# Kernel tuning notes

Hardware: AMD Instinct MI355X
Metric: run time of the kernel (lower is better)

## Reference

```python
import jax, jax.numpy as jnp
import numpy as np

B, D, H, C, T = 65536, 512, 256, 100, 10
EPS = 0.01  # halt_epsilon


def setup_inputs() -> dict:
    key = jax.random.key(0)
    ks = jax.random.split(key, 10)
    sD = 1.0 / np.sqrt(D)
    sH = 1.0 / np.sqrt(H)
    return {
        "x": jax.random.normal(ks[0], (B, D), dtype=jnp.float32),
        # GRUCell params (PyTorch layout: rows chunked as [r; z; n])
        "W_ih": jax.random.uniform(ks[1], (3 * H, D), minval=-sD, maxval=sD, dtype=jnp.float32),
        "W_hh": jax.random.uniform(ks[2], (3 * H, H), minval=-sH, maxval=sH, dtype=jnp.float32),
        "b_ih": jax.random.uniform(ks[3], (3 * H,), minval=-sH, maxval=sH, dtype=jnp.float32),
        "b_hh": jax.random.uniform(ks[4], (3 * H,), minval=-sH, maxval=sH, dtype=jnp.float32),
        # halting unit
        "W_halt": jax.random.uniform(ks[5], (1, H), minval=-sH, maxval=sH, dtype=jnp.float32),
        "b_halt": jax.random.uniform(ks[6], (1,), minval=-sH, maxval=sH, dtype=jnp.float32),
        # readout
        "W_ro": jax.random.uniform(ks[7], (C, H), minval=-sH, maxval=sH, dtype=jnp.float32),
        "b_ro": jax.random.uniform(ks[8], (C,), minval=-sH, maxval=sH, dtype=jnp.float32),
    }


def _act_forward(x, W_ih, W_hh, b_ih, b_hh, W_halt, b_halt, W_ro, b_ro):
    dt = x.dtype
    thresh = jnp.asarray(1.0 - EPS, dt)
    # x is static across ponder steps -> precompute input projection once
    x_proj = x @ W_ih.T + b_ih                       # [B, 3H]
    xr, xz, xn = jnp.split(x_proj, 3, axis=-1)

    def step(carry, _):
        h, cum, rem, nup, acc = carry
        h_proj = h @ W_hh.T + b_hh                   # [B, 3H]
        hr, hz, hn = jnp.split(h_proj, 3, axis=-1)
        r = jax.nn.sigmoid(xr + hr)
        z = jax.nn.sigmoid(xz + hz)
        n = jnp.tanh(xn + r * hn)
        h_new = (1.0 - z) * n + z * h                # GRUCell update
        halt = jax.nn.sigmoid(h_new @ W_halt.T + b_halt)[:, 0]  # [B]
        logits_t = h_new @ W_ro.T + b_ro             # [B, C]
        still = (cum < thresh).astype(dt)
        new_halt = halt * still
        would = (cum + new_halt > thresh).astype(dt)
        remainder = (1.0 - cum) * would * still
        step_w = new_halt * (1.0 - would) + remainder
        cum2 = cum + step_w
        acc2 = acc + step_w[:, None] * h_new
        return (h_new, cum2, rem + remainder, nup + still, acc2), (h_new, halt, logits_t)

    zB = jnp.zeros((x.shape[0],), dt)
    init = (jnp.zeros((x.shape[0], W_hh.shape[1]), dt), zB, zB, zB,
            jnp.zeros((x.shape[0], W_hh.shape[1]), dt))
    (h, cum, remainders, n_updates, acc), (h_seq, halt_seq, logits_seq) = jax.lax.scan(
        step, init, None, length=T)
    logits = acc @ W_ro.T + b_ro                     # [B, C]
    ponder_cost = n_updates.mean() + remainders.mean()
    # scan stacks on axis 0 (time) -> move to dim 1 as torch.stack(dim=1)
    h_seq = jnp.swapaxes(h_seq, 0, 1)                # [B, T, H]
    halt_seq = jnp.swapaxes(halt_seq, 0, 1)          # [B, T]
    logits_seq = jnp.swapaxes(logits_seq, 0, 1)      # [B, T, C]
    return logits, ponder_cost, n_updates, h_seq, halt_seq, logits_seq


def reference(x, W_ih, W_hh, b_ih, b_hh, W_halt, b_halt, W_ro, b_ro):
    return _act_forward(x, W_ih, W_hh, b_ih, b_hh, W_halt, b_halt, W_ro, b_ro)
```

## Files before the change

kernel.cpp:

```cpp
#include <hip/hip_runtime.h>
#include <cmath>


namespace {
constexpr int B = 65536, D = 512, H = 256, C = 100, T = 10;

constexpr long OUT_LOGITS = 0;
constexpr long OUT_PONDER = (long)B * C;
constexpr long OUT_NUP    = OUT_PONDER + 1;
constexpr long OUT_HSEQ   = OUT_NUP + B;
constexpr long OUT_HALT   = OUT_HSEQ + (long)B * T * H;
constexpr long OUT_LSEQ   = OUT_HALT + (long)B * T;

constexpr long NIH  = 768L * D;
constexpr long NHH  = 768L * H;
constexpr long NAUG = 112L * H;

constexpr long WS_XP   = 0;
constexpr long WS_W16  = WS_XP + (long)B * 768;
constexpr long W_HALV  = 2 * (NIH + NHH + NAUG);
constexpr long WS_HL   = WS_W16 + (W_HALV + 1) / 2;
constexpr long WS_HP4  = WS_HL + (long)B * T;
constexpr long WS_NUPB = WS_HP4 + 4L * B * T;
constexpr long WS_REMB = WS_NUPB + B;
constexpr long WS_H16  = WS_REMB + B;
constexpr long H16_PER_T = 1024L * 32768;

constexpr float SC  = 256.f;
constexpr float ISC = 1.f / 256.f;
constexpr float SB  = 1.f / 65536.f;
}

typedef __attribute__((ext_vector_type(8))) _Float16 h8;
typedef __attribute__((ext_vector_type(4))) _Float16 h4;
typedef __attribute__((ext_vector_type(4))) float f4;

#define MFMA16(A, Bo, Cc) __builtin_amdgcn_mfma_f32_16x16x32_f16(A, Bo, Cc, 0, 0, 0)
#define PROD3(a, Ah, Al, Bh, Bl)                                               \
  a = MFMA16(Al, Bh, a);                                                       \
  a = MFMA16(Ah, Bl, a);                                                       \
  a = MFMA16(Ah, Bh, a);

__device__ __forceinline__ float sigmoidf_(float x) {
  if (x >= 0.f) { return 1.f / (1.f + expf(-x)); }
  float e = expf(x);
  return e / (1.f + e);
}

__device__ __forceinline__ void gload_lds16(const _Float16* g, _Float16* l) {
  __builtin_amdgcn_global_load_lds(
      (const __attribute__((address_space(1))) unsigned int*)g,
      (__attribute__((address_space(3))) unsigned int*)l, 16, 0, 0);
}

__global__ void k_prep(const float* __restrict__ wih_s, const float* __restrict__ whh_s,
                       const float* __restrict__ wro, const float* __restrict__ whalt,
                       _Float16* __restrict__ wr) {
  long idx = (long)blockIdx.x * 256 + threadIdx.x;
  if (idx < NIH) {
    float xs = wih_s[idx] * SC;
    _Float16 h = (_Float16)xs;
    _Float16 l = (_Float16)(xs - (float)h);
    wr[idx] = h; wr[NIH + idx] = l;
  }
  if (idx < NHH) {
    float xs = whh_s[idx] * SC;
    _Float16 h = (_Float16)xs;
    _Float16 l = (_Float16)(xs - (float)h);
    long b = 2 * NIH;
    wr[b + idx] = h; wr[b + NHH + idx] = l;
  }
  if (idx < NAUG) {
    int row = (int)(idx >> 8), k = (int)(idx & 255);
    float x = (row < C) ? wro[row * 256 + k] : ((row == C) ? whalt[k] : 0.f);
    float xs = x * SC;
    _Float16 h = (_Float16)xs;
    _Float16 l = (_Float16)(xs - (float)h);
    long b = 2 * (NIH + NHH);
    wr[b + idx] = h; wr[b + NAUG + idx] = l;
  }
}

__device__ __forceinline__ void stageA16(const float* __restrict__ src,
                                         _Float16* As0, _Float16* As1,
                                         int o) {
#pragma unroll
  for (int i = 0; i < 4; ++i) {
    float4 v = ((const float4*)src)[i];
    float vv[4] = {v.x, v.y, v.z, v.w};
    h4 hh, ll;
#pragma unroll
    for (int c = 0; c < 4; ++c) {
      float sv = vv[c] * SC;
      _Float16 h = (_Float16)sv;
      hh[c] = h;
      ll[c] = (_Float16)(sv - (float)h);
    }
    *(h4*)&As0[o + i * 4] = hh;
    *(h4*)&As1[o + i * 4] = ll;
  }
}

__global__ __launch_bounds__(256, 3) void k_xproj(
    const float* __restrict__ x, const _Float16* __restrict__ wih,
    const float* __restrict__ b_ih, float* __restrict__ xpt) {
  __shared__ __align__(16) _Float16 As0[128 * 40], As1[128 * 40];
  __shared__ __align__(16) _Float16 Bs[2][192 * 32];
  const int tid = threadIdx.x;
  const int w = tid >> 6, l = tid & 63;
  const int lr = l & 15, lq = l >> 4;
  const int bid = blockIdx.x;
  const int gid = (bid & 7) * 256 + (bid >> 3);
  const int c0 = (gid & 3) * 64;
  const int rb = (gid >> 2) * 128;

  f4 acc[8][3];
#pragma unroll
  for (int i = 0; i < 8; ++i)
#pragma unroll
    for (int g = 0; g < 3; ++g) acc[i][g] = (f4)0.f;

  for (int kc = 0; kc < 16; ++kc) {
    const int k0 = kc * 32;
    __syncthreads();
    {
      const int row = tid >> 1, kk0 = (tid & 1) * 16;
      stageA16(x + (long)(rb + row) * D + k0 + kk0, As0, As1, row * 40 + kk0);
    }
#pragma unroll
    for (int j = 0; j < 6; ++j) {
      int chunk = w * 6 + j;
      int plane = chunk / 12;
      int rem = chunk - plane * 12;
      int scol = rem * 16 + (l >> 2);
      int kq = l & 3;
      int gcol = (scol >> 6) * 256 + c0 + (scol & 63);
      gload_lds16(wih + (long)plane * NIH + (long)gcol * D + k0 + kq * 8,
                  &Bs[plane][rem * 512]);
    }
    __syncthreads();
    h8 Bh[3], Bl[3];
#pragma unroll
    for (int g = 0; g < 3; ++g) {
      Bh[g] = *(const h8*)&Bs[0][(g * 64 + w * 16 + lr) * 32 + lq * 8];
      Bl[g] = *(const h8*)&Bs[1][(g * 64 + w * 16 + lr) * 32 + lq * 8];
    }
#pragma unroll
    for (int i = 0; i < 8; ++i) {
      h8 Ah = *(const h8*)&As0[(i * 16 + lr) * 40 + lq * 8];
      h8 Al = *(const h8*)&As1[(i * 16 + lr) * 40 + lq * 8];
#pragma unroll
      for (int g = 0; g < 3; ++g) { PROD3(acc[i][g], Ah, Al, Bh[g], Bl[g]); }
    }
  }
  const int ch = c0 + w * 16 + lr;
  const int strip = gid & 3;
  float bi[3] = {b_ih[ch], b_ih[256 + ch], b_ih[512 + ch]};
  const long xoff = (long)(lq * 256 + w * 64 + lr * 4);
#pragma unroll
  for (int i = 0; i < 8; ++i) {
    const long t4s = (long)((gid >> 2) * 2 + (i >> 2)) * 4 + strip;
#pragma unroll
    for (int g = 0; g < 3; ++g) {
      float4 v = make_float4(fmaf(acc[i][g][0], SB, bi[g]),
                             fmaf(acc[i][g][1], SB, bi[g]),
                             fmaf(acc[i][g][2], SB, bi[g]),
                             fmaf(acc[i][g][3], SB, bi[g]));
      *(float4*)&xpt[((t4s * 3 + g) * 4 + (i & 3)) * 1024 + xoff] = v;
    }
  }
}

__global__ __launch_bounds__(256, 4) void k_gru(
    const _Float16* __restrict__ whh, const float* __restrict__ xpt,
    const float* __restrict__ b_hh, const float* __restrict__ w_halt,
    float* __restrict__ out, _Float16* __restrict__ h16,
    float* __restrict__ hp4, int t) {
  __shared__ __align__(16) char uSmem[32768];
  _Float16* AsBuf = (_Float16*)uSmem;
  float*    hseqS = (float*)uSmem;
  _Float16* h16S  = (_Float16*)(uSmem + 16384);
  __shared__ float lds_hp[64][4];
  const int tid = threadIdx.x;
  const int w = tid >> 6, l = tid & 63;
  const int lr = l & 15, lq = l >> 4;
  const int bid = blockIdx.x;
  const int gid = (bid & 7) * 512 + (bid >> 3);
  const int strip = gid & 3;
  const int c0 = strip * 64;
  const int rb = (gid >> 2) * 64;
  const long tilebase = (long)(rb >> 6) * 32768;
  const int ch = c0 + w * 16 + lr;
  const int kc_h = ch >> 5;

  const float bhr = b_hh[ch], bhz = b_hh[256 + ch], bhn = b_hh[512 + ch];
  const float whv = w_halt[ch];

  f4 acc[4][3];
  float ho[4][4];
  float xnv[4][4];
  const long t4s = (long)(gid >> 2) * 4 + strip;
  const long xoff = (long)(lq * 256 + w * 64 + lr * 4);
#pragma unroll
  for (int i = 0; i < 4; ++i) {
    float4 vr = *(const float4*)&xpt[((t4s * 3 + 0) * 4 + i) * 1024 + xoff];
    float4 vz = *(const float4*)&xpt[((t4s * 3 + 1) * 4 + i) * 1024 + xoff];
    float4 vn = *(const float4*)&xpt[((t4s * 3 + 2) * 4 + i) * 1024 + xoff];
    acc[i][0][0] = vr.x * 65536.f; acc[i][0][1] = vr.y * 65536.f;
    acc[i][0][2] = vr.z * 65536.f; acc[i][0][3] = vr.w * 65536.f;
    acc[i][1][0] = vz.x * 65536.f; acc[i][1][1] = vz.y * 65536.f;
    acc[i][1][2] = vz.z * 65536.f; acc[i][1][3] = vz.w * 65536.f;
    xnv[i][0] = vn.x; xnv[i][1] = vn.y; xnv[i][2] = vn.z; xnv[i][3] = vn.w;
    acc[i][2] = (f4)0.f;
#pragma unroll
    for (int reg = 0; reg < 4; ++reg) ho[i][reg] = 0.f;
  }

  if (t > 0) {
    const _Float16* h16r = h16 + (long)(t - 1) * H16_PER_T + tilebase;

#define STAGE_A(buf, kc_)                                                       \
    {                                                                           \
      _Pragma("unroll")                                                         \
      for (int j = 0; j < 2; ++j) {                                             \
        int c = w * 2 + j;                                                      \
        int plane = c >> 2, cc = c & 3;                                         \
        gload_lds16(h16r + (long)(kc_) * 4096 + plane * 2048 + cc * 512 + l * 8,\
                    AsBuf + (buf) * 4096 + plane * 2048 + cc * 512);            \
      }                                                                         \
    }

    STAGE_A(0, 0);
    int cur = 0;
#pragma unroll
    for (int kc = 0; kc < 8; ++kc) {
      const int k0 = kc * 32;
      __builtin_amdgcn_s_barrier();
      h8 Bh[3], Bl[3];
#pragma unroll
      for (int g = 0; g < 3; ++g) {
        Bh[g] = *(const h8*)(whh + (long)(g * 256 + ch) * H + k0 + lq * 8);
        Bl[g] = *(const h8*)(whh + NHH + (long)(g * 256 + ch) * H + k0 + lq * 8);
      }
      __builtin_amdgcn_sched_barrier(0);
      if (kc < 7) STAGE_A(cur ^ 1, kc + 1);
      asm volatile("s_waitcnt vmcnt(2)" ::: "memory");
      __builtin_amdgcn_s_barrier();
      __builtin_amdgcn_sched_barrier(0);
#pragma unroll
      for (int i = 0; i < 4; ++i) {
        h8 Ah = *(const h8*)&AsBuf[cur * 4096 + (i * 16 + lr) * 32 + lq * 8];
        h8 Al = *(const h8*)&AsBuf[cur * 4096 + 2048 + (i * 16 + lr) * 32 + lq * 8];
#pragma unroll
        for (int g = 0; g < 3; ++g) { PROD3(acc[i][g], Ah, Al, Bh[g], Bl[g]); }
      }
      if (kc == kc_h) {
#pragma unroll
        for (int i = 0; i < 4; ++i)
#pragma unroll
          for (int reg = 0; reg < 4; ++reg) {
            int rloc = i * 16 + lq * 4 + reg;
            ho[i][reg] = ((float)AsBuf[cur * 4096 + rloc * 32 + (ch & 31)] +
                          (float)AsBuf[cur * 4096 + 2048 + rloc * 32 + (ch & 31)]) * ISC;
          }
      }
      cur ^= 1;
    }
#undef STAGE_A
  }

  float hvv[4][4];
#pragma unroll
  for (int i = 0; i < 4; ++i)
#pragma unroll
    for (int reg = 0; reg < 4; ++reg) {
      float rr = sigmoidf_(fmaf(acc[i][0][reg], SB, bhr));
      float zz = sigmoidf_(fmaf(acc[i][1][reg], SB, bhz));
      float nn = tanhf(xnv[i][reg] + rr * fmaf(acc[i][2][reg], SB, bhn));
      hvv[i][reg] = (1.f - zz) * nn + zz * ho[i][reg];
    }

  __syncthreads();

  const int kcl = w >> 1;
  const int kk = (w & 1) * 16 + lr;
#pragma unroll
  for (int i = 0; i < 4; ++i)
#pragma unroll
    for (int reg = 0; reg < 4; ++reg) {
      const int rloc = i * 16 + lq * 4 + reg;
      const float hv = hvv[i][reg];
      hseqS[rloc * 64 + w * 16 + lr] = hv;
      float sv = hv * SC;
      _Float16 hi = (_Float16)sv;
      _Float16 lo = (_Float16)(sv - (float)hi);
      h16S[(kcl * 2 + 0) * 2048 + rloc * 32 + kk] = hi;
      h16S[(kcl * 2 + 1) * 2048 + rloc * 32 + kk] = lo;
      float p = hv * whv;
#pragma unroll
      for (int m = 1; m < 16; m <<= 1) p += __shfl_xor(p, m, 64);
      if (lr == 0) lds_hp[rloc][w] = p;
    }
  __syncthreads();

#pragma unroll
  for (int k = 0; k < 4; ++k) {
    int cid = k * 256 + tid;
    int row = cid >> 4, ch16 = cid & 15;
    *(float4*)&out[OUT_HSEQ + (long)(rb + row) * (T * H) + (long)t * H + c0 + ch16 * 4] =
        *(const float4*)&hseqS[row * 64 + ch16 * 4];
  }
  {
    _Float16* dst = h16 + (long)t * H16_PER_T + tilebase + (long)(2 * strip) * 4096;
#pragma unroll
    for (int k = 0; k < 4; ++k) {
      int cid = k * 256 + tid;
      *(float4*)&dst[cid * 8] = *(const float4*)&h16S[cid * 8];
    }
  }
  if (tid < 64)
    hp4[((long)t * 4 + strip) * B + rb + tid] =
        ((lds_hp[tid][0] + lds_hp[tid][1]) + (lds_hp[tid][2] + lds_hp[tid][3]));
}

__global__ __launch_bounds__(256, 4) void k_lseq(
    const _Float16* __restrict__ h16, const _Float16* __restrict__ waug,
    const float* __restrict__ b_ro, float* __restrict__ lseq) {
  __shared__ __align__(16) _Float16 As[128 * 32];
  __shared__ __align__(16) _Float16 Bs[112 * 32];
  const int tid = threadIdx.x;
  const int w = tid >> 6, l = tid & 63;
  const int lr = l & 15, lq = l >> 4;
  const int t = blockIdx.x >> 9;
  const int btile = blockIdx.x & 511;
  const _Float16* h16r = h16 + (long)t * H16_PER_T + (long)btile * 65536;

  f4 acc[2][7];
#pragma unroll
  for (int i = 0; i < 2; ++i)
#pragma unroll
    for (int j = 0; j < 7; ++j) acc[i][j] = (f4)0.f;

  for (int kc = 0; kc < 8; ++kc) {
    const int k0 = kc * 32;
    __syncthreads();
#pragma unroll
    for (int j = 0; j < 2; ++j) {
      int c = w * 2 + j;
      gload_lds16(h16r + (long)(c >> 2) * 32768 + (long)kc * 4096 + (c & 3) * 512 + l * 8,
                  &As[c * 512]);
    }
#pragma unroll
    for (int j = 0; j < 2; ++j) {
      int chunk = w + j * 4;
      if (chunk < 7) {
        int scol = chunk * 16 + (l >> 2);
        int kq = l & 3;
        gload_lds16(waug + (long)scol * H + k0 + kq * 8, &Bs[chunk * 512]);
      }
    }
    __syncthreads();
    h8 Af[2];
#pragma unroll
    for (int i = 0; i < 2; ++i)
      Af[i] = *(const h8*)&As[(w * 32 + i * 16 + lr) * 32 + lq * 8];
#pragma unroll
    for (int j = 0; j < 7; ++j) {
      h8 Bf = *(const h8*)&Bs[(j * 16 + lr) * 32 + lq * 8];
#pragma unroll
      for (int i = 0; i < 2; ++i) acc[i][j] = MFMA16(Af[i], Bf, acc[i][j]);
    }
  }
#pragma unroll
  for (int j = 0; j < 7; ++j) {
    const int col = j * 16 + lr;
    if (col < C) {
      const float br = b_ro[col];
#pragma unroll
      for (int i = 0; i < 2; ++i)
#pragma unroll
        for (int reg = 0; reg < 4; ++reg) {
          long b = (long)btile * 128 + w * 32 + i * 16 + lq * 4 + reg;
          lseq[(b * T + t) * C + col] = fmaf(acc[i][j][reg], SB, br);
        }
    }
  }
}

__global__ void k_act(const float* __restrict__ hp4, const float* __restrict__ b_halt,
                      float* __restrict__ out, float* __restrict__ swb,
                      float* __restrict__ nupb, float* __restrict__ remb) {
  const long b = (long)blockIdx.x * 256 + threadIdx.x;
  const float bh = b_halt[0];
  float cum = 0.f, rem = 0.f, nu = 0.f;
#pragma unroll
  for (int t = 0; t < T; ++t) {
    float v = bh + hp4[((long)t * 4 + 0) * B + b] + hp4[((long)t * 4 + 1) * B + b] +
              hp4[((long)t * 4 + 2) * B + b] + hp4[((long)t * 4 + 3) * B + b];
    float halt = sigmoidf_(v);
    out[OUT_HALT + b * T + t] = halt;
    float still = (cum < 0.99f) ? 1.f : 0.f;
    float nh = halt * still;
    float would = ((cum + nh) > 0.99f) ? 1.f : 0.f;
    float rema = (1.f - cum) * would * still;
    float swv = nh * (1.f - would) + rema;
    cum += swv; rem += rema; nu += still;
    swb[b * T + t] = swv;
  }
  nupb[b] = nu; remb[b] = rem;
}

__global__ void k_logits(const float* __restrict__ lseq, const float* __restrict__ swb,
                         const float* __restrict__ b_ro, const float* __restrict__ nupb,
                         float* __restrict__ out) {
  const long b = blockIdx.x;
  const int tid = threadIdx.x;
  if (tid < C) {
    float br = b_ro[tid];
    float s = br;
#pragma unroll
    for (int t = 0; t < T; ++t) {
      float sw = swb[b * T + t];
      s = fmaf(sw, lseq[(b * T + t) * C + tid] - br, s);
    }
    out[OUT_LOGITS + b * C + tid] = s;
  } else if (tid == C) {
    out[OUT_NUP + b] = nupb[b];
  }
}

__global__ void k_ponder(const float* __restrict__ nupb, const float* __restrict__ remb,
                         float* __restrict__ out) {
  __shared__ float sm[4];
  float s = 0.f;
  for (int i = threadIdx.x; i < B; i += 256) s += nupb[i] + remb[i];
#pragma unroll
  for (int m = 1; m < 64; m <<= 1) s += __shfl_xor(s, m, 64);
  int w = threadIdx.x >> 6;
  if ((threadIdx.x & 63) == 0) sm[w] = s;
  __syncthreads();
  if (threadIdx.x == 0)
    out[OUT_PONDER] = (sm[0] + sm[1] + sm[2] + sm[3]) * (1.f / (float)B);
}

extern "C" void kernel_launch(void* const* d_in, const int* in_sizes, int n_in,
                              void* d_out, int out_size, void* d_ws, size_t ws_size,
                              hipStream_t stream) {
  const float* x      = (const float*)d_in[0];
  const float* W_ih   = (const float*)d_in[1];
  const float* W_hh   = (const float*)d_in[2];
  const float* b_ih   = (const float*)d_in[3];
  const float* b_hh   = (const float*)d_in[4];
  const float* W_halt = (const float*)d_in[5];
  const float* b_halt = (const float*)d_in[6];
  const float* W_ro   = (const float*)d_in[7];
  const float* b_ro   = (const float*)d_in[8];
  float* out = (float*)d_out;
  float* ws  = (float*)d_ws;

  float* xpt       = ws + WS_XP;
  _Float16* w16    = (_Float16*)(ws + WS_W16);
  _Float16* wih16  = w16;
  _Float16* whh16  = w16 + 2 * NIH;
  _Float16* waug16 = w16 + 2 * (NIH + NHH);
  float* swb  = ws + WS_HL;
  float* hp4  = ws + WS_HP4;
  float* nupb = ws + WS_NUPB;
  float* remb = ws + WS_REMB;
  _Float16* h16 = (_Float16*)(ws + WS_H16);

  k_prep<<<(int)((NIH + 255) / 256), 256, 0, stream>>>(W_ih, W_hh, W_ro, W_halt, w16);
  k_xproj<<<2048, 256, 0, stream>>>(x, wih16, b_ih, xpt);
  for (int t = 0; t < T; ++t)
    k_gru<<<4096, 256, 0, stream>>>(whh16, xpt, b_hh, W_halt, out, h16, hp4, t);
  k_lseq<<<512 * T, 256, 0, stream>>>(h16, waug16, b_ro, out + OUT_LSEQ);
  k_act<<<B / 256, 256, 0, stream>>>(hp4, b_halt, out, swb, nupb, remb);
  k_logits<<<B, 128, 0, stream>>>(out + OUT_LSEQ, swb, b_ro, nupb, out);
  k_ponder<<<1, 256, 0, stream>>>(nupb, remb, out);
}
```

Before: 2.405 ms.

## Load recurrent h operand directly from global instead of LDS double-buffering

```diff
diff --git a/kernel.cpp b/kernel.cpp
--- a/kernel.cpp
+++ b/kernel.cpp
@@ -177,7 +177,6 @@
     float* __restrict__ out, _Float16* __restrict__ h16,
     float* __restrict__ hp4, int t) {
   __shared__ __align__(16) char uSmem[32768];
-  _Float16* AsBuf = (_Float16*)uSmem;
   float*    hseqS = (float*)uSmem;
   _Float16* h16S  = (_Float16*)(uSmem + 16384);
   __shared__ float lds_hp[64][4];
@@ -197,90 +196,72 @@
   const float whv = w_halt[ch];
 
   f4 acc[4][3];
-  float ho[4][4];
-  float xnv[4][4];
   const long t4s = (long)(gid >> 2) * 4 + strip;
   const long xoff = (long)(lq * 256 + w * 64 + lr * 4);
 #pragma unroll
   for (int i = 0; i < 4; ++i) {
     float4 vr = *(const float4*)&xpt[((t4s * 3 + 0) * 4 + i) * 1024 + xoff];
     float4 vz = *(const float4*)&xpt[((t4s * 3 + 1) * 4 + i) * 1024 + xoff];
-    float4 vn = *(const float4*)&xpt[((t4s * 3 + 2) * 4 + i) * 1024 + xoff];
     acc[i][0][0] = vr.x * 65536.f; acc[i][0][1] = vr.y * 65536.f;
     acc[i][0][2] = vr.z * 65536.f; acc[i][0][3] = vr.w * 65536.f;
     acc[i][1][0] = vz.x * 65536.f; acc[i][1][1] = vz.y * 65536.f;
     acc[i][1][2] = vz.z * 65536.f; acc[i][1][3] = vz.w * 65536.f;
-    xnv[i][0] = vn.x; xnv[i][1] = vn.y; xnv[i][2] = vn.z; xnv[i][3] = vn.w;
     acc[i][2] = (f4)0.f;
-#pragma unroll
-    for (int reg = 0; reg < 4; ++reg) ho[i][reg] = 0.f;
-  }
-
+  }
+
+  const _Float16* h16r = h16 + (long)(t - 1) * H16_PER_T + tilebase;
   if (t > 0) {
-    const _Float16* h16r = h16 + (long)(t - 1) * H16_PER_T + tilebase;
-
-#define STAGE_A(buf, kc_)                                                       \
-    {                                                                           \
-      _Pragma("unroll")                                                         \
-      for (int j = 0; j < 2; ++j) {                                             \
-        int c = w * 2 + j;                                                      \
-        int plane = c >> 2, cc = c & 3;                                         \
-        gload_lds16(h16r + (long)(kc_) * 4096 + plane * 2048 + cc * 512 + l * 8,\
-                    AsBuf + (buf) * 4096 + plane * 2048 + cc * 512);            \
-      }                                                                         \
-    }
-
-    STAGE_A(0, 0);
-    int cur = 0;
 #pragma unroll
     for (int kc = 0; kc < 8; ++kc) {
       const int k0 = kc * 32;
-      __builtin_amdgcn_s_barrier();
-      h8 Bh[3], Bl[3];
+      h8 Ah[4], Al[4], Bh[3], Bl[3];
+#pragma unroll
+      for (int i = 0; i < 4; ++i) {
+        Ah[i] = *(const h8*)(h16r + (long)kc * 4096 + (i * 16 + lr) * 32 + lq * 8);
+        Al[i] = *(const h8*)(h16r + (long)kc * 4096 + 2048 + (i * 16 + lr) * 32 + lq * 8);
+      }
 #pragma unroll
       for (int g = 0; g < 3; ++g) {
         Bh[g] = *(const h8*)(whh + (long)(g * 256 + ch) * H + k0 + lq * 8);
         Bl[g] = *(const h8*)(whh + NHH + (long)(g * 256 + ch) * H + k0 + lq * 8);
       }
-      __builtin_amdgcn_sched_barrier(0);
-      if (kc < 7) STAGE_A(cur ^ 1, kc + 1);
-      asm volatile("s_waitcnt vmcnt(2)" ::: "memory");
-      __builtin_amdgcn_s_barrier();
-      __builtin_amdgcn_sched_barrier(0);
-#pragma unroll
-      for (int i = 0; i < 4; ++i) {
-        h8 Ah = *(const h8*)&AsBuf[cur * 4096 + (i * 16 + lr) * 32 + lq * 8];
-        h8 Al = *(const h8*)&AsBuf[cur * 4096 + 2048 + (i * 16 + lr) * 32 + lq * 8];
-#pragma unroll
-        for (int g = 0; g < 3; ++g) { PROD3(acc[i][g], Ah, Al, Bh[g], Bl[g]); }
+#pragma unroll
+      for (int i = 0; i < 4; ++i)
+#pragma unroll
+        for (int g = 0; g < 3; ++g) { PROD3(acc[i][g], Ah[i], Al[i], Bh[g], Bl[g]); }
+    }
+  }
+
+  float ho[4][4];
+  if (t > 0) {
+    const _Float16* hoP0 = h16r + (long)kc_h * 4096 + (ch & 31);
+#pragma unroll
+    for (int i = 0; i < 4; ++i)
+#pragma unroll
+      for (int reg = 0; reg < 4; ++reg) {
+        int rloc = i * 16 + lq * 4 + reg;
+        ho[i][reg] = ((float)hoP0[rloc * 32] + (float)hoP0[2048 + rloc * 32]) * ISC;
       }
-      if (kc == kc_h) {
-#pragma unroll
-        for (int i = 0; i < 4; ++i)
-#pragma unroll
-          for (int reg = 0; reg < 4; ++reg) {
-            int rloc = i * 16 + lq * 4 + reg;
-            ho[i][reg] = ((float)AsBuf[cur * 4096 + rloc * 32 + (ch & 31)] +
-                          (float)AsBuf[cur * 4096 + 2048 + rloc * 32 + (ch & 31)]) * ISC;
-          }
-      }
-      cur ^= 1;
-    }
-#undef STAGE_A
+  } else {
+#pragma unroll
+    for (int i = 0; i < 4; ++i)
+#pragma unroll
+      for (int reg = 0; reg < 4; ++reg) ho[i][reg] = 0.f;
   }
 
   float hvv[4][4];
 #pragma unroll
-  for (int i = 0; i < 4; ++i)
+  for (int i = 0; i < 4; ++i) {
+    float4 vn = *(const float4*)&xpt[((t4s * 3 + 2) * 4 + i) * 1024 + xoff];
+    float xnv[4] = {vn.x, vn.y, vn.z, vn.w};
 #pragma unroll
     for (int reg = 0; reg < 4; ++reg) {
       float rr = sigmoidf_(fmaf(acc[i][0][reg], SB, bhr));
       float zz = sigmoidf_(fmaf(acc[i][1][reg], SB, bhz));
-      float nn = tanhf(xnv[i][reg] + rr * fmaf(acc[i][2][reg], SB, bhn));
+      float nn = tanhf(xnv[reg] + rr * fmaf(acc[i][2][reg], SB, bhn));
       hvv[i][reg] = (1.f - zz) * nn + zz * ho[i][reg];
     }
-
-  __syncthreads();
+  }
 
   const int kcl = w >> 1;
   const int kk = (w & 1) * 16 + lr;
```

New measurement: 2.674 ms. 11.2% more time.
